# Optimization experiments

Measured on AMD Instinct MI355X. Metric: run time of the kernel, lower is better.

The kernel has to match this reference:

```python
import jax, jax.numpy as jnp
import numpy as np

B, D, H, O = 4096, 1024, 8192, 1000

def setup_inputs() -> dict:
    key = jax.random.key(0)
    k1, k2, k3 = jax.random.split(key, 3)
    x = jax.random.normal(k1, (B, D), dtype=jnp.float32)
    kohonen_weights = jax.random.normal(k2, (H, D), dtype=jnp.float32) * (6.0 / (H + D)) ** 0.5
    grossberg_weights = jax.random.normal(k3, (O, H), dtype=jnp.float32) * (6.0 / (O + H)) ** 0.5
    return {"x": x, "kohonen_weights": kohonen_weights, "grossberg_weights": grossberg_weights}

def reference(x, kohonen_weights, grossberg_weights):
    # but kept faithful since distances only feed argmin -> same winners either way)
    x_sq = jnp.sum(x * x, axis=1, keepdims=True)                      # [B,1]
    w_sq = jnp.sum(kohonen_weights * kohonen_weights, axis=1)         # [H]
    sq_dists = x_sq - 2.0 * (x @ kohonen_weights.T) + w_sq[None, :]   # [B,H]
    winners = jnp.argmin(sq_dists, axis=1)                            # [B]
    # one_hot @ grossberg.T is mathematically a row gather of grossberg.T
    output = grossberg_weights.T[winners]                             # [B,O]
    return output, winners
```

## Files before the change

### kernel.cpp

```cpp
#include <hip/hip_runtime.h>
#include <hip/hip_bf16.h>

#define B_ 4096
#define D_ 1024
#define H_ 8192
#define O_ 1000
#define K2 2048
#define NT 48
#define NITER (NT / 2)

typedef __attribute__((ext_vector_type(8))) short short8;
typedef __attribute__((ext_vector_type(4))) short short4v;
typedef __attribute__((ext_vector_type(4))) float f32x4;

union BF4 { __hip_bfloat16 b[4]; short4v s; };

__device__ __forceinline__ void gload16(void* ldsp, const void* g) {
  __builtin_amdgcn_global_load_lds(
      (const __attribute__((address_space(1))) unsigned int*)g,
      (__attribute__((address_space(3))) unsigned int*)ldsp, 16, 0, 0);
}

__device__ __forceinline__ int aoff_(int T) {
  const int t = T / 3, r = T - 3 * t;
  return (r == 1 ? 1024 : 0) + t * 64;
}
__device__ __forceinline__ int boff_(int T) {
  const int t = T / 3, r = T - 3 * t;
  return (r == 2 ? 1024 : 0) + t * 64;
}

__global__ __launch_bounds__(256) void split_rows_kernel(
    const float* __restrict__ src, __hip_bfloat16* __restrict__ dst,
    float* __restrict__ sq)
{
  const int r = blockIdx.x;
  const int t = threadIdx.x;
  const float4 v = ((const float4*)(src + (size_t)r * D_))[t];
  float ss = v.x * v.x + v.y * v.y + v.z * v.z + v.w * v.w;

  BF4 Hh, Ll;
  const float e[4] = {v.x, v.y, v.z, v.w};
#pragma unroll
  for (int i = 0; i < 4; ++i) {
    __hip_bfloat16 h = __float2bfloat16(e[i]);
    Hh.b[i] = h;
    Ll.b[i] = __float2bfloat16(e[i] - __bfloat162float(h));
  }
  __hip_bfloat16* base = dst + (size_t)r * K2;
  *(short4v*)(base + t * 4) = Hh.s;
  *(short4v*)(base + 1024 + t * 4) = Ll.s;

#pragma unroll
  for (int o = 32; o > 0; o >>= 1) ss += __shfl_down(ss, o);
  __shared__ float wsum[4];
  if ((t & 63) == 0) wsum[t >> 6] = ss;
  __syncthreads();
  if (t == 0) sq[r] = (wsum[0] + wsum[1]) + (wsum[2] + wsum[3]);
}


#define BAR() do { asm volatile("" ::: "memory"); \
                   __builtin_amdgcn_s_barrier(); \
                   asm volatile("" ::: "memory"); } while (0)
#define SB0() __builtin_amdgcn_sched_barrier(0)
#define GATEV0() asm volatile("s_waitcnt vmcnt(0)" ::: "memory")

#define STAGE(P, prow, T, isB, h) do { if ((T) < NT) { \
    const int koff_ = (isB) ? boff_(T) : aoff_(T); \
    const __hip_bfloat16* s_ = (P) + (size_t)((prow) + (h)*128 + wid*16 + srow) * K2 + koff_ + sunit * 8; \
    char* d_ = lds + ((T)&1)*65536 + (isB)*32768 + (h)*16384 + wid*2048 + lane*16; \
    gload16(d_, s_); gload16(d_ + 1024, s_ + 8*K2); } } while (0)

#define READ_A(dst, dsel, mh, KOF) do { \
    const char* p_ = lds + (dsel) + wm*16384 + (mh)*8192 + aro + (KOF); \
    _Pragma("unroll") for (int m_ = 0; m_ < 4; ++m_) \
      dst[m_] = *(const short8*)(p_ + m_*2048); } while (0)

#define READ_B(dst, dsel, KOF) do { \
    const char* p_ = lds + (dsel) + 32768 + bq + aro + (KOF); \
    _Pragma("unroll") for (int n_ = 0; n_ < 4; ++n_) \
      dst[n_] = *(const short8*)(p_ + n_*2048); } while (0)

#define MM16(mh, AF, BF) do { \
    __builtin_amdgcn_s_setprio(1); \
    _Pragma("unroll") for (int m_ = 0; m_ < 4; ++m_) \
    _Pragma("unroll") for (int n_ = 0; n_ < 4; ++n_) \
      acc[(mh)*4 + m_][n_] = __builtin_amdgcn_mfma_f32_16x16x32_bf16( \
          AF[m_], BF[n_], acc[(mh)*4 + m_][n_], 0, 0, 0); \
    __builtin_amdgcn_s_setprio(0); } while (0)

__global__ __launch_bounds__(512, 2) void gemm_argmin_kernel(
    const __hip_bfloat16* __restrict__ Ap, const __hip_bfloat16* __restrict__ Bp,
    const float* __restrict__ xsq, const float* __restrict__ wsq,
    unsigned long long* __restrict__ keys)
{
  __shared__ char lds[131072];

  const int t = threadIdx.x;
  const int id = blockIdx.x;
  const int xcd = id & 7;
  const int r_ = id >> 3;
  const int by = (xcd >> 2) * 8 + (r_ >> 3);
  const int bx = (xcd & 3) * 8 + (r_ & 7);
  const int brow = by * 256, bcol = bx * 256;

  const int lane = t & 63, wid = t >> 6;
  const int wm = wid >> 2, wn = wid & 3;
  const int cc = lane & 15, q = lane >> 4, sw = lane & 7;
  const int aro = cc * 128;
  const int kof0 = (q ^ sw) * 16;
  const int kof1 = ((4 + q) ^ sw) * 16;
  const int bq = (wn >> 1) * 16384 + (wn & 1) * 8192;

  const int srow = lane >> 3;
  const int sunit = (lane & 7) ^ srow;

  f32x4 acc[8][4] = {};
  short8 afA[4], afB[4], bfA[4], bfB[4];

  STAGE(Ap, brow, 0, 0, 0); STAGE(Ap, brow, 0, 0, 1);
  STAGE(Bp, bcol, 0, 1, 0); STAGE(Bp, bcol, 0, 1, 1);
  STAGE(Bp, bcol, 1, 1, 0); STAGE(Bp, bcol, 1, 1, 1);
  asm volatile("s_waitcnt vmcnt(4)" ::: "memory");
  BAR();
  READ_A(afA, 0, 0, kof0);
  READ_B(bfA, 0, kof0);

  for (int it = 0; it < NITER; ++it) {
    const int a = 2 * it, b = 2 * it + 1;
    STAGE(Ap, brow, b, 0, 0); STAGE(Ap, brow, b, 0, 1);
    READ_A(afB, 0, 1, kof0);
    SB0();
    MM16(0, afA, bfA);
    BAR();
    READ_A(afA, 0, 0, kof1);
    READ_B(bfB, 0, kof1);
    SB0();
    MM16(1, afB, bfA);
    BAR();
    READ_A(afB, 0, 1, kof1);
    SB0();
    MM16(0, afA, bfB);
    GATEV0();
    BAR();
    STAGE(Bp, bcol, a + 2, 1, 0);
    READ_A(afA, 65536, 0, kof0);
    READ_B(bfA, 65536, kof0);
    SB0();
    MM16(1, afB, bfB);
    BAR();
    STAGE(Bp, bcol, a + 2, 1, 1);
    STAGE(Ap, brow, a + 2, 0, 0); STAGE(Ap, brow, a + 2, 0, 1);
    READ_A(afB, 65536, 1, kof0);
    SB0();
    MM16(0, afA, bfA);
    BAR();
    READ_A(afA, 65536, 0, kof1);
    READ_B(bfB, 65536, kof1);
    SB0();
    MM16(1, afB, bfA);
    BAR();
    READ_A(afB, 65536, 1, kof1);
    SB0();
    MM16(0, afA, bfB);
    GATEV0();
    BAR();
    STAGE(Bp, bcol, b + 2, 1, 0); STAGE(Bp, bcol, b + 2, 1, 1);
    if (it < NITER - 1) {
      READ_A(afA, 0, 0, kof0);
      READ_B(bfA, 0, kof0);
    }
    SB0();
    MM16(1, afB, bfB);
    BAR();
  }

#pragma unroll
  for (int m = 0; m < 8; ++m) {
#pragma unroll
    for (int r = 0; r < 4; ++r) {
      const int row = brow + wm * 128 + m * 16 + q * 4 + r;
      const float xs = xsq[row];
      unsigned long long best = ~0ULL;
#pragma unroll
      for (int n = 0; n < 4; ++n) {
        const int col = bcol + wn * 64 + n * 16 + cc;
        const float s = (xs - 2.0f * acc[m][n][r]) + wsq[col];
        unsigned ub = __float_as_uint(s);
        ub = (ub & 0x80000000u) ? ~ub : (ub | 0x80000000u);
        const unsigned long long key =
            ((unsigned long long)ub << 32) | (unsigned)col;
        if (key < best) best = key;
      }
#pragma unroll
      for (int o = 1; o < 16; o <<= 1) {
        const unsigned long long v = __shfl_xor(best, o);
        if (v < best) best = v;
      }
      if (cc == 0) atomicMin(&keys[row], best);
    }
  }
}

__global__ __launch_bounds__(256) void transposeG_kernel(
    const float* __restrict__ G, float* __restrict__ GT)
{
  __shared__ float tile[32][33];
  const int h0 = blockIdx.x * 32;
  const int o0 = blockIdx.y * 32;
  const int tx = threadIdx.x;
  const int ty = threadIdx.y;
#pragma unroll
  for (int j = 0; j < 4; ++j) {
    const int o = o0 + ty + j * 8;
    if (o < O_) tile[ty + j * 8][tx] = G[(size_t)o * H_ + h0 + tx];
  }
  __syncthreads();
  const int o = o0 + tx;
  if (o < O_) {
#pragma unroll
    for (int j = 0; j < 4; ++j)
      GT[(size_t)(h0 + ty + j * 8) * O_ + o] = tile[tx][ty + j * 8];
  }
}

__global__ __launch_bounds__(256) void finalize_kernel(
    const unsigned long long* __restrict__ keys,
    const float* __restrict__ GT, float* __restrict__ out)
{
  const int b = blockIdx.x;
  const unsigned w = (unsigned)(keys[b] & 0xFFFFFFFFull);
  if (threadIdx.x == 0) out[(size_t)B_ * O_ + b] = (float)w;
  const float4* src = (const float4*)(GT + (size_t)w * O_);
  float4* dst = (float4*)(out + (size_t)b * O_);
  for (int i = threadIdx.x; i < O_ / 4; i += 256) dst[i] = src[i];
}

extern "C" void kernel_launch(void* const* d_in, const int* in_sizes, int n_in,
                              void* d_out, int out_size, void* d_ws, size_t ws_size,
                              hipStream_t stream)
{
  (void)in_sizes; (void)n_in; (void)out_size; (void)ws_size;
  const float* x = (const float*)d_in[0];
  const float* kw = (const float*)d_in[1];
  const float* gw = (const float*)d_in[2];
  float* out = (float*)d_out;

  char* ws = (char*)d_ws;
  __hip_bfloat16* Ap = (__hip_bfloat16*)(ws);
  __hip_bfloat16* Bp = (__hip_bfloat16*)(ws + 16777216);
  float* xsq = (float*)(ws + 50331648);
  float* wsq = (float*)(ws + 50331648 + 16384);
  unsigned long long* keys = (unsigned long long*)(ws + 50331648 + 16384 + 32768);
  float* GT = (float*)(ws);

  hipMemsetAsync(keys, 0xFF, B_ * sizeof(unsigned long long), stream);
  split_rows_kernel<<<B_, 256, 0, stream>>>(x, Ap, xsq);
  split_rows_kernel<<<H_, 256, 0, stream>>>(kw, Bp, wsq);
  gemm_argmin_kernel<<<512, 512, 0, stream>>>(Ap, Bp, xsq, wsq, keys);
  transposeG_kernel<<<dim3(H_ / 32, (O_ + 31) / 32), dim3(32, 8), 0, stream>>>(gw, GT);
  finalize_kernel<<<B_, 256, 0, stream>>>(keys, GT, out);
}
```

Before: 249.1 us.

## Restructure GEMM main loop into quadrant MFMA phases with partial vmcnt gating

Rewrites the GEMM K-loop so each wave loads full-K fragments (both k halves) for a 4x2 sub-tile and issues MFMAs per (mh,nh) quadrant. Global-to-LDS staging is spread one stage per phase and gated with vmcnt(8) instead of vmcnt(0), which keeps more loads in flight. The warp-to-tile mapping changes to match, and the epilogue row/col indexing is updated. It also fuses the two split kernels and the memset into a single launch. Together these aim to cut exposed load latency and launch overhead, at the risk of LDS buffer hazards if the gating is off, and more fragment registers.

```diff
diff --git a/kernel.cpp b/kernel.cpp
--- a/kernel.cpp
+++ b/kernel.cpp
@@ -30,13 +30,25 @@
   return (r == 2 ? 1024 : 0) + t * 64;
 }
 
-__global__ __launch_bounds__(256) void split_rows_kernel(
-    const float* __restrict__ src, __hip_bfloat16* __restrict__ dst,
-    float* __restrict__ sq)
+__global__ __launch_bounds__(256) void split_all_kernel(
+    const float* __restrict__ x, const float* __restrict__ w,
+    __hip_bfloat16* __restrict__ Ap, __hip_bfloat16* __restrict__ Bp,
+    float* __restrict__ xsq, float* __restrict__ wsq,
+    unsigned long long* __restrict__ keys)
 {
   const int r = blockIdx.x;
   const int t = threadIdx.x;
-  const float4 v = ((const float4*)(src + (size_t)r * D_))[t];
+  const float* src;
+  __hip_bfloat16* dst;
+  float* sq;
+  if (r < B_) {
+    src = x + (size_t)r * D_; dst = Ap + (size_t)r * K2; sq = xsq + r;
+    if (t == 0) keys[r] = ~0ULL;
+  } else {
+    const int rr = r - B_;
+    src = w + (size_t)rr * D_; dst = Bp + (size_t)rr * K2; sq = wsq + rr;
+  }
+  const float4 v = ((const float4*)src)[t];
   float ss = v.x * v.x + v.y * v.y + v.z * v.z + v.w * v.w;
 
   BF4 Hh, Ll;
@@ -47,24 +59,22 @@
     Hh.b[i] = h;
     Ll.b[i] = __float2bfloat16(e[i] - __bfloat162float(h));
   }
-  __hip_bfloat16* base = dst + (size_t)r * K2;
-  *(short4v*)(base + t * 4) = Hh.s;
-  *(short4v*)(base + 1024 + t * 4) = Ll.s;
+  *(short4v*)(dst + t * 4) = Hh.s;
+  *(short4v*)(dst + 1024 + t * 4) = Ll.s;
 
 #pragma unroll
   for (int o = 32; o > 0; o >>= 1) ss += __shfl_down(ss, o);
   __shared__ float wsum[4];
   if ((t & 63) == 0) wsum[t >> 6] = ss;
   __syncthreads();
-  if (t == 0) sq[r] = (wsum[0] + wsum[1]) + (wsum[2] + wsum[3]);
+  if (t == 0) *sq = (wsum[0] + wsum[1]) + (wsum[2] + wsum[3]);
 }
 
 
 #define BAR() do { asm volatile("" ::: "memory"); \
                    __builtin_amdgcn_s_barrier(); \
                    asm volatile("" ::: "memory"); } while (0)
-#define SB0() __builtin_amdgcn_sched_barrier(0)
-#define GATEV0() asm volatile("s_waitcnt vmcnt(0)" ::: "memory")
+#define GATE8() asm volatile("s_waitcnt vmcnt(8)" ::: "memory")
 
 #define STAGE(P, prow, T, isB, h) do { if ((T) < NT) { \
     const int koff_ = (isB) ? boff_(T) : aoff_(T); \
@@ -72,22 +82,25 @@
     char* d_ = lds + ((T)&1)*65536 + (isB)*32768 + (h)*16384 + wid*2048 + lane*16; \
     gload16(d_, s_); gload16(d_ + 1024, s_ + 8*K2); } } while (0)
 
-#define READ_A(dst, dsel, mh, KOF) do { \
-    const char* p_ = lds + (dsel) + wm*16384 + (mh)*8192 + aro + (KOF); \
-    _Pragma("unroll") for (int m_ = 0; m_ < 4; ++m_) \
-      dst[m_] = *(const short8*)(p_ + m_*2048); } while (0)
-
-#define READ_B(dst, dsel, KOF) do { \
-    const char* p_ = lds + (dsel) + 32768 + bq + aro + (KOF); \
-    _Pragma("unroll") for (int n_ = 0; n_ < 4; ++n_) \
-      dst[n_] = *(const short8*)(p_ + n_*2048); } while (0)
-
-#define MM16(mh, AF, BF) do { \
+#define READ_A(dst, db, mh) do { \
+    const char* p_ = lds + (db) + (mh)*16384 + (wm*64 + cc)*128; \
+    _Pragma("unroll") for (int m_ = 0; m_ < 4; ++m_) { \
+      dst[2*m_]   = *(const short8*)(p_ + m_*2048 + kof0); \
+      dst[2*m_+1] = *(const short8*)(p_ + m_*2048 + kof1); } } while (0)
+
+#define READ_B(dst, db, nh) do { \
+    const char* p_ = lds + (db) + 32768 + (nh)*16384 + (wn*32 + cc)*128; \
+    _Pragma("unroll") for (int n_ = 0; n_ < 2; ++n_) { \
+      dst[2*n_]   = *(const short8*)(p_ + n_*2048 + kof0); \
+      dst[2*n_+1] = *(const short8*)(p_ + n_*2048 + kof1); } } while (0)
+
+#define MM(mh, nh, AF, BF) do { \
     __builtin_amdgcn_s_setprio(1); \
     _Pragma("unroll") for (int m_ = 0; m_ < 4; ++m_) \
-    _Pragma("unroll") for (int n_ = 0; n_ < 4; ++n_) \
-      acc[(mh)*4 + m_][n_] = __builtin_amdgcn_mfma_f32_16x16x32_bf16( \
-          AF[m_], BF[n_], acc[(mh)*4 + m_][n_], 0, 0, 0); \
+    _Pragma("unroll") for (int n_ = 0; n_ < 2; ++n_) \
+    _Pragma("unroll") for (int kk = 0; kk < 2; ++kk) \
+      acc[(mh)*4+m_][(nh)*2+n_] = __builtin_amdgcn_mfma_f32_16x16x32_bf16( \
+          AF[2*m_+kk], BF[2*n_+kk], acc[(mh)*4+m_][(nh)*2+n_], 0, 0, 0); \
     __builtin_amdgcn_s_setprio(0); } while (0)
 
 __global__ __launch_bounds__(512, 2) void gemm_argmin_kernel(
@@ -108,85 +121,78 @@
   const int lane = t & 63, wid = t >> 6;
   const int wm = wid >> 2, wn = wid & 3;
   const int cc = lane & 15, q = lane >> 4, sw = lane & 7;
-  const int aro = cc * 128;
   const int kof0 = (q ^ sw) * 16;
   const int kof1 = ((4 + q) ^ sw) * 16;
-  const int bq = (wn >> 1) * 16384 + (wn & 1) * 8192;
 
   const int srow = lane >> 3;
   const int sunit = (lane & 7) ^ srow;
 
   f32x4 acc[8][4] = {};
-  short8 afA[4], afB[4], bfA[4], bfB[4];
-
-  STAGE(Ap, brow, 0, 0, 0); STAGE(Ap, brow, 0, 0, 1);
-  STAGE(Bp, bcol, 0, 1, 0); STAGE(Bp, bcol, 0, 1, 1);
-  STAGE(Bp, bcol, 1, 1, 0); STAGE(Bp, bcol, 1, 1, 1);
-  asm volatile("s_waitcnt vmcnt(4)" ::: "memory");
+  short8 aF0[8], aF1[8], bF0[4], bF1[4];
+
+  STAGE(Ap, brow, 0, 0, 0);
+  STAGE(Bp, bcol, 0, 1, 0);
+  STAGE(Bp, bcol, 0, 1, 1);
+  STAGE(Ap, brow, 0, 0, 1);
+  STAGE(Ap, brow, 1, 0, 0);
+  STAGE(Bp, bcol, 1, 1, 0);
+  STAGE(Bp, bcol, 1, 1, 1);
+  GATE8();
   BAR();
-  READ_A(afA, 0, 0, kof0);
-  READ_B(bfA, 0, kof0);
+  READ_A(aF0, 0, 0);
+  READ_B(bF0, 0, 0);
 
   for (int it = 0; it < NITER; ++it) {
-    const int a = 2 * it, b = 2 * it + 1;
-    STAGE(Ap, brow, b, 0, 0); STAGE(Ap, brow, b, 0, 1);
-    READ_A(afB, 0, 1, kof0);
-    SB0();
-    MM16(0, afA, bfA);
-    BAR();
-    READ_A(afA, 0, 0, kof1);
-    READ_B(bfB, 0, kof1);
-    SB0();
-    MM16(1, afB, bfA);
-    BAR();
-    READ_A(afB, 0, 1, kof1);
-    SB0();
-    MM16(0, afA, bfB);
-    GATEV0();
+    const int a = 2 * it, b = a + 1;
+    READ_B(bF1, 0, 1);
+    STAGE(Ap, brow, b, 0, 1);
+    MM(0, 0, aF0, bF0);
+    GATE8(); BAR();
+    READ_A(aF1, 0, 1);
+    STAGE(Ap, brow, a + 2, 0, 0);
+    MM(0, 1, aF0, bF1);
     BAR();
     STAGE(Bp, bcol, a + 2, 1, 0);
-    READ_A(afA, 65536, 0, kof0);
-    READ_B(bfA, 65536, kof0);
-    SB0();
-    MM16(1, afB, bfB);
+    MM(1, 0, aF1, bF0);
+    GATE8(); BAR();
+    READ_A(aF0, 65536, 0);
+    READ_B(bF0, 65536, 0);
+    STAGE(Bp, bcol, a + 2, 1, 1);
+    MM(1, 1, aF1, bF1);
+    GATE8(); BAR();
+    READ_B(bF1, 65536, 1);
+    STAGE(Ap, brow, a + 2, 0, 1);
+    MM(0, 0, aF0, bF0);
+    GATE8(); BAR();
+    READ_A(aF1, 65536, 1);
+    STAGE(Ap, brow, b + 2, 0, 0);
+    MM(0, 1, aF0, bF1);
     BAR();
-    STAGE(Bp, bcol, a + 2, 1, 1);
-    STAGE(Ap, brow, a + 2, 0, 0); STAGE(Ap, brow, a + 2, 0, 1);
-    READ_A(afB, 65536, 1, kof0);
-    SB0();
-    MM16(0, afA, bfA);
-    BAR();
-    READ_A(afA, 65536, 0, kof1);
-    READ_B(bfB, 65536, kof1);
-    SB0();
-    MM16(1, afB, bfA);
-    BAR();
-    READ_A(afB, 65536, 1, kof1);
-    SB0();
-    MM16(0, afA, bfB);
-    GATEV0();
-    BAR();
-    STAGE(Bp, bcol, b + 2, 1, 0); STAGE(Bp, bcol, b + 2, 1, 1);
-    if (it < NITER - 1) {
-      READ_A(afA, 0, 0, kof0);
-      READ_B(bfA, 0, kof0);
+    STAGE(Bp, bcol, b + 2, 1, 0);
+    MM(1, 0, aF1, bF0);
+    GATE8(); BAR();
+    if (it + 1 < NITER) {
+      READ_A(aF0, 0, 0);
+      READ_B(bF0, 0, 0);
     }
-    SB0();
-    MM16(1, afB, bfB);
-    BAR();
-  }
-
-#pragma unroll
-  for (int m = 0; m < 8; ++m) {
+    STAGE(Bp, bcol, b + 2, 1, 1);
+    MM(1, 1, aF1, bF1);
+    GATE8(); BAR();
+  }
+
+#pragma unroll
+  for (int i = 0; i < 8; ++i) {
+    const int mh = i >> 2, m_ = i & 3;
 #pragma unroll
     for (int r = 0; r < 4; ++r) {
-      const int row = brow + wm * 128 + m * 16 + q * 4 + r;
+      const int row = brow + mh * 128 + wm * 64 + m_ * 16 + q * 4 + r;
       const float xs = xsq[row];
       unsigned long long best = ~0ULL;
 #pragma unroll
-      for (int n = 0; n < 4; ++n) {
-        const int col = bcol + wn * 64 + n * 16 + cc;
-        const float s = (xs - 2.0f * acc[m][n][r]) + wsq[col];
+      for (int j = 0; j < 4; ++j) {
+        const int nh = j >> 1, n_ = j & 1;
+        const int col = bcol + nh * 128 + wn * 32 + n_ * 16 + cc;
+        const float s = (xs - 2.0f * acc[i][j][r]) + wsq[col];
         unsigned ub = __float_as_uint(s);
         ub = (ub & 0x80000000u) ? ~ub : (ub | 0x80000000u);
         const unsigned long long key =
@@ -255,9 +261,7 @@
   unsigned long long* keys = (unsigned long long*)(ws + 50331648 + 16384 + 32768);
   float* GT = (float*)(ws);
 
-  hipMemsetAsync(keys, 0xFF, B_ * sizeof(unsigned long long), stream);
-  split_rows_kernel<<<B_, 256, 0, stream>>>(x, Ap, xsq);
-  split_rows_kernel<<<H_, 256, 0, stream>>>(kw, Bp, wsq);
+  split_all_kernel<<<B_ + H_, 256, 0, stream>>>(x, kw, Ap, Bp, xsq, wsq, keys);
   gemm_argmin_kernel<<<512, 512, 0, stream>>>(Ap, Bp, xsq, wsq, keys);
   transposeG_kernel<<<dim3(H_ / 32, (O_ + 31) / 32), dim3(32, 8), 0, stream>>>(gw, GT);
   finalize_kernel<<<B_, 256, 0, stream>>>(keys, GT, out);
```

After: 280.8 us. +12.7%, slower.
